# Kernel optimization log

Hardware: AMD Instinct MI355X
Metric: run time of the kernel (lower is better)

## Reference

```python
import jax, jax.numpy as jnp
import numpy as np

POOL_SIZE = 7
NUM_ROIS = 1000
H, W, C = 128, 128, 1024


def setup_inputs() -> dict:
    key = jax.random.key(0)
    k_img, k_xy, k_wh = jax.random.split(key, 3)
    img = jax.random.normal(k_img, (1, H, W, C), dtype=jnp.float32)
    # rois[0, i] = (x, y, w, h) in feature-map pixel units; ensure x+w<=W, y+h<=H
    xy = jax.random.randint(k_xy, (1, NUM_ROIS, 2), 0, 64, dtype=jnp.int32)
    wh = jax.random.randint(k_wh, (1, NUM_ROIS, 2), 8, 65, dtype=jnp.int32)
    rois = jnp.concatenate([xy, wh], axis=-1)  # [1, num_rois, 4]
    return {"img": img, "rois": rois}


def _axis_coords(start, size, out_size):
    """Half-pixel-center bilinear source coords for a crop [start, start+size).

    Matches tf.image.resize(method='bilinear', antialias=False): src = (i+0.5)*scale - 0.5,
    clamped to the crop, then split into floor index / +1 index / lerp weight.
    """
    size_f = size.astype(jnp.float32)
    f = (jnp.arange(out_size, dtype=jnp.float32) + 0.5) * (size_f / out_size) - 0.5
    f = jnp.clip(f, 0.0, jnp.maximum(size_f - 1.0, 0.0))
    i0 = jnp.floor(f).astype(jnp.int32)
    i1 = jnp.minimum(i0 + 1, size - 1)
    wgt = f - i0.astype(jnp.float32)
    return start + i0, start + i1, wgt


def _pool_one_roi(img2d, roi):
    # img2d: [H, W, C]; roi: [4] int32 (x, y, w, h)
    x, y, w, h = roi[0], roi[1], roi[2], roi[3]
    y0, y1, wy = _axis_coords(y, h, POOL_SIZE)  # each [P]
    x0, x1, wx = _axis_coords(x, w, POOL_SIZE)
    v00 = img2d[y0[:, None], x0[None, :], :]  # [P, P, C]
    v01 = img2d[y0[:, None], x1[None, :], :]
    v10 = img2d[y1[:, None], x0[None, :], :]
    v11 = img2d[y1[:, None], x1[None, :], :]
    wy = wy[:, None, None]
    wx = wx[None, :, None]
    top = v00 * (1.0 - wx) + v01 * wx
    bot = v10 * (1.0 - wx) + v11 * wx
    return top * (1.0 - wy) + bot * wy


def reference(img, rois):
    # Vectorized RoiPoolingConv.call: batched crop + bilinear resize over all ROIs.
    pooled = jax.vmap(_pool_one_roi, in_axes=(None, 0))(img[0], rois[0])  # [R, P, P, C]
    return pooled[None]  # [1, num_rois, P, P, C]
```

## Files before the change

### kernel.cpp

```cpp
#include <hip/hip_runtime.h>

#define POOL 7
#define NROIS 1000
#define NCELLS (NROIS * POOL * POOL)
#define IMG_W 128
#define NCH 1024
#define NXCD 8
#define ROIS_PER_XCD (NROIS / NXCD)
#define CELLS_PER_XCD (ROIS_PER_XCD * 49)

typedef float f4 __attribute__((ext_vector_type(4)));

__global__ __launch_bounds__(256) void roi_pool_kernel(
    const float* __restrict__ img,
    const int* __restrict__ rois,
    float* __restrict__ out)
{
    const unsigned bid  = blockIdx.x;
    const unsigned xcd  = bid & 7u;
    const unsigned slot = bid >> 3;
    const unsigned rloc = slot / 49u;
    const unsigned c49  = slot - rloc * 49u;
    const unsigned roi  = xcd * ROIS_PER_XCD + rloc;
    const unsigned py   = c49 / 7u;
    const unsigned px   = c49 - py * 7u;

    const int4 r = ((const int4*)rois)[roi];
    const int x = r.x, y = r.y, w = r.z, h = r.w;

    const float hf = (float)h;
    float fy = ((float)py + 0.5f) * (hf / (float)POOL) - 0.5f;
    fy = fminf(fmaxf(fy, 0.0f), fmaxf(hf - 1.0f, 0.0f));
    const int   iy0 = (int)floorf(fy);
    const int   iy1 = min(iy0 + 1, h - 1);
    const float wy  = fy - (float)iy0;
    const int   y0  = y + iy0;
    const int   y1  = y + iy1;

    const float wf = (float)w;
    float fx = ((float)px + 0.5f) * (wf / (float)POOL) - 0.5f;
    fx = fminf(fmaxf(fx, 0.0f), fmaxf(wf - 1.0f, 0.0f));
    const int   ix0 = (int)floorf(fx);
    const int   ix1 = min(ix0 + 1, w - 1);
    const float wx  = fx - (float)ix0;
    const int   x0  = x + ix0;
    const int   x1  = x + ix1;

    const unsigned choff = threadIdx.x * 4u;
    const unsigned cell  = roi * 49u + c49;

    const f4* p00 = (const f4*)(img + ((size_t)y0 * IMG_W + x0) * NCH + choff);
    const f4* p01 = (const f4*)(img + ((size_t)y0 * IMG_W + x1) * NCH + choff);
    const f4* p10 = (const f4*)(img + ((size_t)y1 * IMG_W + x0) * NCH + choff);
    const f4* p11 = (const f4*)(img + ((size_t)y1 * IMG_W + x1) * NCH + choff);
    f4* po = (f4*)(out + (size_t)cell * NCH + choff);

    const f4 a = *p00;
    const f4 b = *p01;
    const f4 c = *p10;
    const f4 d = *p11;

    const float owx = 1.0f - wx;
    const float owy = 1.0f - wy;

    const f4 top = a * owx + b * wx;
    const f4 bot = c * owx + d * wx;
    const f4 res = top * owy + bot * wy;

    __builtin_nontemporal_store(res, po);
}

extern "C" void kernel_launch(void* const* d_in, const int* in_sizes, int n_in,
                              void* d_out, int out_size, void* d_ws, size_t ws_size,
                              hipStream_t stream)
{
    const float* img  = (const float*)d_in[0];
    const int*   rois = (const int*)d_in[1];
    float*       out  = (float*)d_out;

    const int nblocks = CELLS_PER_XCD * NXCD;
    roi_pool_kernel<<<nblocks, 256, 0, stream>>>(img, rois, out);
}
```

Baseline: 309.2 us.

## Use persistent blocks processing cell chunks with software-pipelined loads

Replaces one-block-per-cell launch with 2048 blocks that each walk a contiguous chunk of 24 cells. The loads for the next cell are issued before the current cell is interpolated and stored. The aim is to cut block launch overhead and keep loads in flight. The cost is fewer resident waves and more registers for the double-buffered values, which may reduce memory-level parallelism.

```diff
diff --git a/kernel.cpp b/kernel.cpp
--- a/kernel.cpp
+++ b/kernel.cpp
@@ -8,22 +8,20 @@
 #define NXCD 8
 #define ROIS_PER_XCD (NROIS / NXCD)
 #define CELLS_PER_XCD (ROIS_PER_XCD * 49)
+#define BLKS_PER_XCD 256
+#define CHUNK 24
 
 typedef float f4 __attribute__((ext_vector_type(4)));
 
-__global__ __launch_bounds__(256) void roi_pool_kernel(
-    const float* __restrict__ img,
-    const int* __restrict__ rois,
-    float* __restrict__ out)
+__device__ __forceinline__ void issue_cell(
+    const float* __restrict__ img, const int* __restrict__ rois,
+    float* __restrict__ out, unsigned cell, unsigned choff,
+    f4& a, f4& b, f4& c, f4& d, float& wx, float& wy, f4*& po)
 {
-    const unsigned bid  = blockIdx.x;
-    const unsigned xcd  = bid & 7u;
-    const unsigned slot = bid >> 3;
-    const unsigned rloc = slot / 49u;
-    const unsigned c49  = slot - rloc * 49u;
-    const unsigned roi  = xcd * ROIS_PER_XCD + rloc;
-    const unsigned py   = c49 / 7u;
-    const unsigned px   = c49 - py * 7u;
+    const unsigned roi = cell / 49u;
+    const unsigned c49 = cell - roi * 49u;
+    const unsigned py  = c49 / 7u;
+    const unsigned px  = c49 - py * 7u;
 
     const int4 r = ((const int4*)rois)[roi];
     const int x = r.x, y = r.y, w = r.z, h = r.w;
@@ -33,7 +31,7 @@
     fy = fminf(fmaxf(fy, 0.0f), fmaxf(hf - 1.0f, 0.0f));
     const int   iy0 = (int)floorf(fy);
     const int   iy1 = min(iy0 + 1, h - 1);
-    const float wy  = fy - (float)iy0;
+    wy = fy - (float)iy0;
     const int   y0  = y + iy0;
     const int   y1  = y + iy1;
 
@@ -42,32 +40,61 @@
     fx = fminf(fmaxf(fx, 0.0f), fmaxf(wf - 1.0f, 0.0f));
     const int   ix0 = (int)floorf(fx);
     const int   ix1 = min(ix0 + 1, w - 1);
-    const float wx  = fx - (float)ix0;
+    wx = fx - (float)ix0;
     const int   x0  = x + ix0;
     const int   x1  = x + ix1;
-
-    const unsigned choff = threadIdx.x * 4u;
-    const unsigned cell  = roi * 49u + c49;
 
     const f4* p00 = (const f4*)(img + ((size_t)y0 * IMG_W + x0) * NCH + choff);
     const f4* p01 = (const f4*)(img + ((size_t)y0 * IMG_W + x1) * NCH + choff);
     const f4* p10 = (const f4*)(img + ((size_t)y1 * IMG_W + x0) * NCH + choff);
     const f4* p11 = (const f4*)(img + ((size_t)y1 * IMG_W + x1) * NCH + choff);
-    f4* po = (f4*)(out + (size_t)cell * NCH + choff);
 
-    const f4 a = *p00;
-    const f4 b = *p01;
-    const f4 c = *p10;
-    const f4 d = *p11;
+    a = *p00;
+    b = *p01;
+    c = *p10;
+    d = *p11;
+    po = (f4*)(out + (size_t)cell * NCH + choff);
+}
 
-    const float owx = 1.0f - wx;
-    const float owy = 1.0f - wy;
+__global__ __launch_bounds__(256) void roi_pool_kernel(
+    const float* __restrict__ img,
+    const int* __restrict__ rois,
+    float* __restrict__ out)
+{
+    const unsigned bid  = blockIdx.x;
+    const unsigned xcd  = bid & 7u;
+    const unsigned blk  = bid >> 3;
 
-    const f4 top = a * owx + b * wx;
-    const f4 bot = c * owx + d * wx;
-    const f4 res = top * owy + bot * wy;
+    const unsigned xbase = xcd * CELLS_PER_XCD;
+    unsigned cc  = xbase + blk * CHUNK;
+    const unsigned end = min(cc + CHUNK, xbase + CELLS_PER_XCD);
+    if (cc >= end) return;
 
-    __builtin_nontemporal_store(res, po);
+    const unsigned choff = threadIdx.x * 4u;
+
+    f4 a, b, c, d; float wx, wy; f4* po;
+    issue_cell(img, rois, out, cc, choff, a, b, c, d, wx, wy, po);
+
+    while (true) {
+        const unsigned cn = cc + 1;
+        const bool more = (cn < end);
+
+        f4 a2, b2, c2, d2; float wx2, wy2; f4* po2;
+        if (more)
+            issue_cell(img, rois, out, cn, choff, a2, b2, c2, d2, wx2, wy2, po2);
+
+        const float owx = 1.0f - wx;
+        const float owy = 1.0f - wy;
+        const f4 top = a * owx + b * wx;
+        const f4 bot = c * owx + d * wx;
+        const f4 res = top * owy + bot * wy;
+        __builtin_nontemporal_store(res, po);
+
+        if (!more) break;
+        a = a2; b = b2; c = c2; d = d2;
+        wx = wx2; wy = wy2; po = po2;
+        cc = cn;
+    }
 }
 
 extern "C" void kernel_launch(void* const* d_in, const int* in_sizes, int n_in,
@@ -78,6 +105,6 @@
     const int*   rois = (const int*)d_in[1];
     float*       out  = (float*)d_out;
 
-    const int nblocks = CELLS_PER_XCD * NXCD;
+    const int nblocks = BLKS_PER_XCD * NXCD;
     roi_pool_kernel<<<nblocks, 256, 0, stream>>>(img, rois, out);
 }
```

Result: slower. 317.2 us (+2.6%).
